# Optimization experiments

Hardware: AMD Instinct MI355X
Metric: run time of the kernel (lower is better)

The kernel has to match this reference:

```python
import jax, jax.numpy as jnp
import numpy as np

N_NODES = 100000
N_EDGES = 3200000
N_FEAT = 512
HIDDEN = 16
N_CLASSES = 40


def gcn_conv(x, src, dst, W, b, num_nodes):
    # GCNConv with self-loops and symmetric normalization (default PyG settings).
    loop = jnp.arange(num_nodes)
    s = jnp.concatenate([src, loop])
    d = jnp.concatenate([dst, loop])
    deg = jax.ops.segment_sum(jnp.ones_like(s, dtype=x.dtype), d, num_segments=num_nodes)
    dinv = jnp.where(deg > 0, jax.lax.rsqrt(deg), 0.0)
    norm = dinv[s] * dinv[d]  # [E+N]
    h = x @ W  # [N, out]
    msg = h[s] * norm[:, None]  # gather + scale
    out = jax.ops.segment_sum(msg, d, num_segments=num_nodes)  # scatter-add
    return out + b


def setup_inputs() -> dict:
    key = jax.random.key(0)
    k1, k2, k3, k4 = jax.random.split(key, 4)
    x = jax.random.normal(k1, (N_NODES, N_FEAT), dtype=jnp.float32)
    edge_index = jax.random.randint(k2, (2, N_EDGES), 0, N_NODES, dtype=jnp.int64)
    W1 = jax.random.normal(k3, (N_FEAT, HIDDEN), dtype=jnp.float32) * 0.05
    b1 = jnp.zeros((HIDDEN,), dtype=jnp.float32)
    W2 = jax.random.normal(k4, (HIDDEN, N_CLASSES), dtype=jnp.float32) * 0.05
    b2 = jnp.zeros((N_CLASSES,), dtype=jnp.float32)
    return {"x": x, "edge_index": edge_index, "W1": W1, "b1": b1, "W2": W2, "b2": b2}


def reference(x, edge_index, W1, b1, W2, b2):
    num_nodes = x.shape[0]
    src, dst = edge_index[0], edge_index[1]
    h = gcn_conv(x, src, dst, W1, b1, num_nodes)
    h = jax.nn.relu(h)
    # dropout is identity in eval mode (training=False)
    out = gcn_conv(h, src, dst, W2, b2, num_nodes)
    return jax.nn.log_softmax(out, axis=1)
```

## Files before the change

kernel.cpp:

```cpp
#include <hip/hip_runtime.h>

#define N_NODES 100000
#define N_EDGES 3200000
#define N_FEAT 512
#define HIDDEN 16
#define N_CLASSES 40

#define SCAN_BLOCKS 98

#define CH3   256
#define NCHK  391
#define NS2   256
#define SLICE2 (N_EDGES / NS2)
#define SL4_2  (SLICE2 / 4)

typedef int v4i __attribute__((ext_vector_type(4)));
typedef int v2i __attribute__((ext_vector_type(2)));

__global__ __launch_bounds__(512) void k_p1b(const int* __restrict__ dst,
                                             int* __restrict__ cnt_sc) {
    __shared__ int hist[NCHK];
    int tid = threadIdx.x;
    int s = blockIdx.x;
    for (int i = tid; i < NCHK; i += 512) hist[i] = 0;
    __syncthreads();
    const v4i* dp = reinterpret_cast<const v4i*>(dst + s * SLICE2);
    for (int i = tid; i < SL4_2; i += 512) {
        v4i d4 = __builtin_nontemporal_load(dp + i);
        atomicAdd(&hist[(unsigned)d4.x >> 8], 1);
        atomicAdd(&hist[(unsigned)d4.y >> 8], 1);
        atomicAdd(&hist[(unsigned)d4.z >> 8], 1);
        atomicAdd(&hist[(unsigned)d4.w >> 8], 1);
    }
    __syncthreads();
    for (int i = tid; i < NCHK; i += 512)
        cnt_sc[s * NCHK + i] = hist[i];
}

__global__ __launch_bounds__(256) void k_scstage2(const int* __restrict__ cnt_sc,
                                                  int* __restrict__ sbase,
                                                  int* __restrict__ tot) {
    int c = blockIdx.x * 4 + (threadIdx.x >> 6);
    int lane = threadIdx.x & 63;
    if (c >= NCHK) return;
    int carry = 0;
    #pragma unroll
    for (int r = 0; r < 4; r++) {
        int s = r * 64 + lane;
        int v = cnt_sc[s * NCHK + c];
        int sc = v;
        #pragma unroll
        for (int off = 1; off < 64; off <<= 1) {
            int t = __shfl_up(sc, off, 64);
            if (lane >= off) sc += t;
        }
        sbase[s * NCHK + c] = carry + sc - v;
        carry += __shfl(sc, 63, 64);
    }
    if (lane == 0) tot[c] = carry;
}

__global__ __launch_bounds__(512) void k_cbscan(const int* __restrict__ tot,
                                                int* __restrict__ cb) {
    int tid = threadIdx.x;
    int v = (tid < NCHK) ? tot[tid] : 0;
    int lane = tid & 63, wv = tid >> 6;
    int sc = v;
    #pragma unroll
    for (int off = 1; off < 64; off <<= 1) {
        int t = __shfl_up(sc, off, 64);
        if (lane >= off) sc += t;
    }
    __shared__ int wsum[8];
    if (lane == 63) wsum[wv] = sc;
    __syncthreads();
    int pre = 0;
    #pragma unroll
    for (int w = 0; w < 8; w++) pre += (w < wv) ? wsum[w] : 0;
    int excl = pre + sc - v;
    if (tid < NCHK) cb[tid] = excl;
    if (tid == NCHK - 1) cb[NCHK] = excl + v;
}

__global__ __launch_bounds__(512) void k_p2stage(const int* __restrict__ src,
                                                 const int* __restrict__ dst,
                                                 const int* __restrict__ sbase,
                                                 const int* __restrict__ cb,
                                                 int2* __restrict__ staged) {
    __shared__ int curpos[NCHK];
    int tid = threadIdx.x;
    int s = blockIdx.x;
    for (int c = tid; c < NCHK; c += 512)
        curpos[c] = cb[c] + sbase[s * NCHK + c];
    __syncthreads();
    const v4i* dp = reinterpret_cast<const v4i*>(dst + s * SLICE2);
    const v4i* sp = reinterpret_cast<const v4i*>(src + s * SLICE2);
    for (int i = tid; i < SL4_2; i += 512) {
        v4i d4 = __builtin_nontemporal_load(dp + i);
        v4i s4 = __builtin_nontemporal_load(sp + i);
        int p0 = atomicAdd(&curpos[(unsigned)d4.x >> 8], 1);
        staged[p0] = make_int2(s4.x, d4.x);
        int p1 = atomicAdd(&curpos[(unsigned)d4.y >> 8], 1);
        staged[p1] = make_int2(s4.y, d4.y);
        int p2 = atomicAdd(&curpos[(unsigned)d4.z >> 8], 1);
        staged[p2] = make_int2(s4.z, d4.z);
        int p3 = atomicAdd(&curpos[(unsigned)d4.w >> 8], 1);
        staged[p3] = make_int2(s4.w, d4.w);
    }
}

__global__ __launch_bounds__(256) void k_deg(const int2* __restrict__ staged,
                                             const int* __restrict__ cb,
                                             int* __restrict__ deg,
                                             float* __restrict__ dinv) {
    __shared__ int cnt[CH3];
    int tid = threadIdx.x;
    int c = blockIdx.x;
    int base = c << 8;
    int lim = N_NODES - base; if (lim > CH3) lim = CH3;
    cnt[tid] = 0;
    __syncthreads();
    int beg = cb[c], end = cb[c + 1];
    const v2i* stp = reinterpret_cast<const v2i*>(staged);
    for (int i = beg + tid; i < end; i += 256) {
        v2i e = stp[i];
        atomicAdd(&cnt[e.y - base], 1);
    }
    __syncthreads();
    if (tid < lim) {
        int d = cnt[tid];
        deg[base + tid] = d;
        dinv[base + tid] = rsqrtf((float)(d + 1));
    }
}


__global__ __launch_bounds__(1024) void k_scan_a(const int* __restrict__ cnt,
                                                 int* __restrict__ bsum) {
    int tid = threadIdx.x;
    int i = blockIdx.x * 1024 + tid;
    int v = (i < N_NODES) ? cnt[i] : 0;
    #pragma unroll
    for (int off = 32; off >= 1; off >>= 1) v += __shfl_xor(v, off, 64);
    __shared__ int ws[16];
    if ((tid & 63) == 0) ws[tid >> 6] = v;
    __syncthreads();
    if (tid == 0) {
        int s = 0;
        #pragma unroll
        for (int w = 0; w < 16; w++) s += ws[w];
        bsum[blockIdx.x] = s;
    }
}

__global__ __launch_bounds__(128) void k_scan_b(const int* __restrict__ bsum,
                                                int* __restrict__ boff) {
    int tid = threadIdx.x;
    int lane = tid & 63, wv = tid >> 6;
    int v = (tid < SCAN_BLOCKS) ? bsum[tid] : 0;
    int sc = v;
    #pragma unroll
    for (int off = 1; off < 64; off <<= 1) {
        int t = __shfl_up(sc, off, 64);
        if (lane >= off) sc += t;
    }
    __shared__ int wsum[2];
    if (lane == 63) wsum[wv] = sc;
    __syncthreads();
    int pre = (wv == 1) ? wsum[0] : 0;
    if (tid < SCAN_BLOCKS) boff[tid] = pre + sc - v;
}

__global__ __launch_bounds__(1024) void k_scan_c(const int* __restrict__ cnt,
                                                 const int* __restrict__ boff,
                                                 int* __restrict__ row_start) {
    int tid = threadIdx.x;
    int i = blockIdx.x * 1024 + tid;
    int lane = tid & 63, wv = tid >> 6;
    int v = (i < N_NODES) ? cnt[i] : 0;
    int sc = v;
    #pragma unroll
    for (int off = 1; off < 64; off <<= 1) {
        int t = __shfl_up(sc, off, 64);
        if (lane >= off) sc += t;
    }
    __shared__ int wsum[16];
    if (lane == 63) wsum[wv] = sc;
    __syncthreads();
    int pre = 0;
    #pragma unroll
    for (int w = 0; w < 16; w++) pre += (w < wv) ? wsum[w] : 0;
    int excl = boff[blockIdx.x] + pre + sc - v;
    if (i < N_NODES) row_start[i] = excl;
    if (i == N_NODES) row_start[N_NODES] = N_EDGES;
}

__global__ __launch_bounds__(512) void k_p3(const int2* __restrict__ staged,
                                            const int* __restrict__ cb,
                                            const int* __restrict__ row_start,
                                            const float* __restrict__ dinv,
                                            int2* __restrict__ edge_data) {
    __shared__ int cur[CH3];
    __shared__ float dv[CH3];
    int tid = threadIdx.x;
    int c = blockIdx.x;
    int base = c << 8;
    int lim = N_NODES - base; if (lim > CH3) lim = CH3;
    if (tid < lim) {
        cur[tid] = row_start[base + tid];
        dv[tid]  = dinv[base + tid];
    }
    __syncthreads();
    int beg = cb[c], end = cb[c + 1];
    const v2i* stp = reinterpret_cast<const v2i*>(staged);
    for (int i = beg + tid; i < end; i += 512) {
        v2i e = __builtin_nontemporal_load(stp + i);
        int nl = e.y - base;
        float nrm = dinv[e.x] * dv[nl];
        int slot = atomicAdd(&cur[nl], 1);
        edge_data[slot] = make_int2(e.x, __float_as_int(nrm));
    }
}


#define KC 32
#define LDSW 36

__global__ __launch_bounds__(256) void k_gemm1(const float* __restrict__ x,
                                               const float* __restrict__ W1,
                                               float* __restrict__ h1) {
    __shared__ float xs[256 * LDSW];
    int tid = threadIdx.x;
    int row = blockIdx.x * 256 + tid;

    float acc[HIDDEN];
    #pragma unroll
    for (int j = 0; j < HIDDEN; j++) acc[j] = 0.f;

    int s_sub = tid >> 3;
    int s_k4  = tid & 7;

    for (int kc = 0; kc < N_FEAT; kc += KC) {
        __syncthreads();
        #pragma unroll
        for (int l = 0; l < 8; l++) {
            int srow = s_sub + l * 32;
            int grow = blockIdx.x * 256 + srow;
            int gr = grow < N_NODES ? grow : N_NODES - 1;
            float4 v = *reinterpret_cast<const float4*>(
                x + (size_t)gr * N_FEAT + kc + s_k4 * 4);
            *reinterpret_cast<float4*>(&xs[srow * LDSW + s_k4 * 4]) = v;
        }
        __syncthreads();

        const float* Wc = W1 + kc * HIDDEN;
        #pragma unroll
        for (int k4 = 0; k4 < 8; k4++) {
            float4 xv = *reinterpret_cast<const float4*>(&xs[tid * LDSW + k4 * 4]);
            const float* w0 = Wc + (k4 * 4 + 0) * HIDDEN;
            const float* w1 = Wc + (k4 * 4 + 1) * HIDDEN;
            const float* w2 = Wc + (k4 * 4 + 2) * HIDDEN;
            const float* w3 = Wc + (k4 * 4 + 3) * HIDDEN;
            #pragma unroll
            for (int j = 0; j < HIDDEN; j++) {
                acc[j] += xv.x * w0[j];
                acc[j] += xv.y * w1[j];
                acc[j] += xv.z * w2[j];
                acc[j] += xv.w * w3[j];
            }
        }
    }

    if (row < N_NODES) {
        float4* op = reinterpret_cast<float4*>(h1 + (size_t)row * HIDDEN);
        #pragma unroll
        for (int q = 0; q < 4; q++)
            op[q] = make_float4(acc[q*4+0], acc[q*4+1], acc[q*4+2], acc[q*4+3]);
    }
}


template <bool RELU>
__global__ __launch_bounds__(256) void k_aggw(const int2* __restrict__ edge_data,
                                              const int* __restrict__ row_start,
                                              const float* __restrict__ dinv,
                                              const float* __restrict__ h,
                                              const float* __restrict__ bias,
                                              float* __restrict__ out) {
    int lane = threadIdx.x & 63;
    int node = blockIdx.x * 4 + (threadIdx.x >> 6);
    int sub = lane >> 4, j = lane & 15;
    int beg = row_start[node], end = row_start[node + 1];
    float ds = dinv[node];
    float acc = (sub == 0) ? h[(size_t)node * HIDDEN + j] * (ds * ds) : 0.f;
    int i = beg + sub;
    for (; i + 12 < end; i += 16) {
        int2 ea = edge_data[i];
        int2 eb = edge_data[i + 4];
        int2 ec = edge_data[i + 8];
        int2 ed = edge_data[i + 12];
        float va = h[(size_t)ea.x * HIDDEN + j];
        float vb = h[(size_t)eb.x * HIDDEN + j];
        float vc = h[(size_t)ec.x * HIDDEN + j];
        float vd = h[(size_t)ed.x * HIDDEN + j];
        acc += va * __int_as_float(ea.y);
        acc += vb * __int_as_float(eb.y);
        acc += vc * __int_as_float(ec.y);
        acc += vd * __int_as_float(ed.y);
    }
    for (; i < end; i += 4) {
        int2 e = edge_data[i];
        acc += h[(size_t)e.x * HIDDEN + j] * __int_as_float(e.y);
    }
    acc += __shfl_xor(acc, 16, 64);
    acc += __shfl_xor(acc, 32, 64);
    if (sub == 0) {
        if (RELU) acc = fmaxf(acc + bias[j], 0.f);
        out[(size_t)node * HIDDEN + j] = acc;
    }
}


__global__ __launch_bounds__(256) void k_out(const float* __restrict__ agg2,
                                             const float* __restrict__ W2,
                                             const float* __restrict__ b2,
                                             float* __restrict__ out) {
    int r = blockIdx.x * 256 + threadIdx.x;
    if (r >= N_NODES) return;
    float a[HIDDEN];
    const float4* ap = reinterpret_cast<const float4*>(agg2 + (size_t)r * HIDDEN);
    #pragma unroll
    for (int q = 0; q < 4; q++) {
        float4 v = ap[q];
        a[q * 4 + 0] = v.x; a[q * 4 + 1] = v.y;
        a[q * 4 + 2] = v.z; a[q * 4 + 3] = v.w;
    }
    float acc[N_CLASSES];
    #pragma unroll
    for (int jj = 0; jj < N_CLASSES; jj++) acc[jj] = b2[jj];
    #pragma unroll
    for (int kk = 0; kk < HIDDEN; kk++) {
        float av = a[kk];
        #pragma unroll
        for (int jj = 0; jj < N_CLASSES; jj++)
            acc[jj] += av * W2[kk * N_CLASSES + jj];
    }
    float m = -1e30f;
    #pragma unroll
    for (int jj = 0; jj < N_CLASSES; jj++) m = fmaxf(m, acc[jj]);
    float sum = 0.f;
    #pragma unroll
    for (int jj = 0; jj < N_CLASSES; jj++) sum += __expf(acc[jj] - m);
    float l = m + __logf(sum);
    float4* op = reinterpret_cast<float4*>(out + (size_t)r * N_CLASSES);
    #pragma unroll
    for (int q = 0; q < N_CLASSES / 4; q++) {
        op[q] = make_float4(acc[q*4+0] - l, acc[q*4+1] - l,
                            acc[q*4+2] - l, acc[q*4+3] - l);
    }
}


extern "C" void kernel_launch(void* const* d_in, const int* in_sizes, int n_in,
                              void* d_out, int out_size, void* d_ws, size_t ws_size,
                              hipStream_t stream) {
    const float* x  = (const float*)d_in[0];
    const int*   ei = (const int*)d_in[1];
    const float* W1 = (const float*)d_in[2];
    const float* b1 = (const float*)d_in[3];
    const float* W2 = (const float*)d_in[4];
    const float* b2 = (const float*)d_in[5];
    const int* src = ei;
    const int* dst = ei + N_EDGES;
    float* out = (float*)d_out;

    char* ws = (char*)d_ws;
    size_t off = 0;
    auto alloc = [&](size_t bytes) {
        size_t o = off; off = (off + bytes + 255) & ~(size_t)255; return o;
    };
    float* dinv      = (float*)(ws + alloc(sizeof(float) * N_NODES));
    int*   cnt       = (int*)  (ws + alloc(sizeof(int) * N_NODES));
    int*   row_start = (int*)  (ws + alloc(sizeof(int) * (N_NODES + 1)));
    int*   cnt_sc    = (int*)  (ws + alloc(sizeof(int) * NS2 * NCHK));
    int*   sbase     = (int*)  (ws + alloc(sizeof(int) * NS2 * NCHK));
    int*   cb        = (int*)  (ws + alloc(sizeof(int) * (NCHK + 1)));
    int*   tot       = (int*)  (ws + alloc(sizeof(int) * NCHK));
    int2*  staged    = (int2*) (ws + alloc(sizeof(int2) * N_EDGES));
    float* h1        = (float*)(ws + off - (size_t)N_EDGES * sizeof(int2));
    float* rbuf      = h1 + (size_t)N_NODES * HIDDEN;
    int2*  edge_data = (int2*) (ws + alloc(sizeof(int2) * N_EDGES));
    float* agg2      = (float*)(ws + alloc(sizeof(float) * N_NODES * HIDDEN));
    int*   bsum      = (int*)  (ws + alloc(sizeof(int) * SCAN_BLOCKS));
    int*   boff      = (int*)  (ws + alloc(sizeof(int) * SCAN_BLOCKS));

    const int nodeBlocks = (N_NODES + 255) / 256;
    const int aggBlocks  = N_NODES / 4;

    k_p1b<<<NS2, 512, 0, stream>>>(dst, cnt_sc);
    k_scstage2<<<(NCHK + 3) / 4, 256, 0, stream>>>(cnt_sc, sbase, tot);
    k_cbscan<<<1, 512, 0, stream>>>(tot, cb);
    k_p2stage<<<NS2, 512, 0, stream>>>(src, dst, sbase, cb, staged);
    k_deg<<<NCHK, 256, 0, stream>>>(staged, cb, cnt, dinv);
    k_scan_a<<<SCAN_BLOCKS, 1024, 0, stream>>>(cnt, bsum);
    k_scan_b<<<1, 128, 0, stream>>>(bsum, boff);
    k_scan_c<<<SCAN_BLOCKS, 1024, 0, stream>>>(cnt, boff, row_start);
    k_p3<<<NCHK, 512, 0, stream>>>(staged, cb, row_start, dinv, edge_data);

    k_gemm1<<<nodeBlocks, 256, 0, stream>>>(x, W1, h1);
    k_aggw<true><<<aggBlocks, 256, 0, stream>>>(edge_data, row_start, dinv, h1, b1, rbuf);
    k_aggw<false><<<aggBlocks, 256, 0, stream>>>(edge_data, row_start, dinv, rbuf, nullptr, agg2);
    k_out<<<nodeBlocks, 256, 0, stream>>>(agg2, W2, b2, out);
}
```

Measured before the change: 571.0 us.

## Fuse CSR-build kernels into one cooperative kernel with grid syncs

Merges the nine graph-preprocessing kernels (histogram, scans, staging, degree, row-start scan, CSR fill) into one cooperative kernel of 256 workgroups, with grid.sync between phases. This removes the launch overhead and inter-kernel gaps of many small kernels. The trade-off is that the degree and CSR-fill phases now run on 256 workgroups looping over 391 chunks instead of 391 blocks, and every grid barrier has its own cost.

```diff
diff --git a/kernel.cpp b/kernel.cpp
--- a/kernel.cpp
+++ b/kernel.cpp
@@ -1,4 +1,7 @@
 #include <hip/hip_runtime.h>
+#include <hip/hip_cooperative_groups.h>
+
+namespace cg = cooperative_groups;
 
 #define N_NODES 100000
 #define N_EDGES 3200000
@@ -6,219 +9,205 @@
 #define HIDDEN 16
 #define N_CLASSES 40
 
-#define SCAN_BLOCKS 98
-
 #define CH3   256
 #define NCHK  391
 #define NS2   256
 #define SLICE2 (N_EDGES / NS2)
 #define SL4_2  (SLICE2 / 4)
+#define RS_WGS 196
 
 typedef int v4i __attribute__((ext_vector_type(4)));
 typedef int v2i __attribute__((ext_vector_type(2)));
 
-__global__ __launch_bounds__(512) void k_p1b(const int* __restrict__ dst,
-                                             int* __restrict__ cnt_sc) {
-    __shared__ int hist[NCHK];
-    int tid = threadIdx.x;
-    int s = blockIdx.x;
-    for (int i = tid; i < NCHK; i += 512) hist[i] = 0;
+__global__ __launch_bounds__(512) void k_build(
+    const int* __restrict__ src, const int* __restrict__ dst,
+    int* __restrict__ cnt_sc, int* __restrict__ sbase, int* __restrict__ tot,
+    int* __restrict__ cb, int* __restrict__ deg, float* __restrict__ dinv,
+    int* __restrict__ bsum, int* __restrict__ boff, int* __restrict__ row_start,
+    int2* __restrict__ staged, int2* __restrict__ edge_data)
+{
+    cg::grid_group grid = cg::this_grid();
+    __shared__ int   sA[NCHK];
+    __shared__ float sB[CH3];
+    const int tid  = threadIdx.x;
+    const int wg   = blockIdx.x;
+    const int lane = tid & 63, wv = tid >> 6;
+
+    for (int i = tid; i < NCHK; i += 512) sA[i] = 0;
     __syncthreads();
-    const v4i* dp = reinterpret_cast<const v4i*>(dst + s * SLICE2);
-    for (int i = tid; i < SL4_2; i += 512) {
-        v4i d4 = __builtin_nontemporal_load(dp + i);
-        atomicAdd(&hist[(unsigned)d4.x >> 8], 1);
-        atomicAdd(&hist[(unsigned)d4.y >> 8], 1);
-        atomicAdd(&hist[(unsigned)d4.z >> 8], 1);
-        atomicAdd(&hist[(unsigned)d4.w >> 8], 1);
-    }
-    __syncthreads();
-    for (int i = tid; i < NCHK; i += 512)
-        cnt_sc[s * NCHK + i] = hist[i];
-}
-
-__global__ __launch_bounds__(256) void k_scstage2(const int* __restrict__ cnt_sc,
-                                                  int* __restrict__ sbase,
-                                                  int* __restrict__ tot) {
-    int c = blockIdx.x * 4 + (threadIdx.x >> 6);
-    int lane = threadIdx.x & 63;
-    if (c >= NCHK) return;
-    int carry = 0;
-    #pragma unroll
-    for (int r = 0; r < 4; r++) {
-        int s = r * 64 + lane;
-        int v = cnt_sc[s * NCHK + c];
+    {
+        const v4i* dp = reinterpret_cast<const v4i*>(dst + wg * SLICE2);
+        for (int i = tid; i < SL4_2; i += 512) {
+            v4i d4 = __builtin_nontemporal_load(dp + i);
+            atomicAdd(&sA[(unsigned)d4.x >> 8], 1);
+            atomicAdd(&sA[(unsigned)d4.y >> 8], 1);
+            atomicAdd(&sA[(unsigned)d4.z >> 8], 1);
+            atomicAdd(&sA[(unsigned)d4.w >> 8], 1);
+        }
+        __syncthreads();
+        for (int i = tid; i < NCHK; i += 512) cnt_sc[wg * NCHK + i] = sA[i];
+    }
+    grid.sync();
+
+    {
+        int c = wg * 8 + wv;
+        if (c < NCHK) {
+            int carry = 0;
+            #pragma unroll
+            for (int r = 0; r < 4; r++) {
+                int s = r * 64 + lane;
+                int v = cnt_sc[s * NCHK + c];
+                int sc = v;
+                #pragma unroll
+                for (int off = 1; off < 64; off <<= 1) {
+                    int t = __shfl_up(sc, off, 64);
+                    if (lane >= off) sc += t;
+                }
+                sbase[s * NCHK + c] = carry + sc - v;
+                carry += __shfl(sc, 63, 64);
+            }
+            if (lane == 0) tot[c] = carry;
+        }
+    }
+    grid.sync();
+
+    if (wg == 0) {
+        int v = (tid < NCHK) ? tot[tid] : 0;
         int sc = v;
         #pragma unroll
         for (int off = 1; off < 64; off <<= 1) {
             int t = __shfl_up(sc, off, 64);
             if (lane >= off) sc += t;
         }
-        sbase[s * NCHK + c] = carry + sc - v;
-        carry += __shfl(sc, 63, 64);
-    }
-    if (lane == 0) tot[c] = carry;
-}
-
-__global__ __launch_bounds__(512) void k_cbscan(const int* __restrict__ tot,
-                                                int* __restrict__ cb) {
-    int tid = threadIdx.x;
-    int v = (tid < NCHK) ? tot[tid] : 0;
-    int lane = tid & 63, wv = tid >> 6;
-    int sc = v;
-    #pragma unroll
-    for (int off = 1; off < 64; off <<= 1) {
-        int t = __shfl_up(sc, off, 64);
-        if (lane >= off) sc += t;
-    }
-    __shared__ int wsum[8];
-    if (lane == 63) wsum[wv] = sc;
-    __syncthreads();
-    int pre = 0;
-    #pragma unroll
-    for (int w = 0; w < 8; w++) pre += (w < wv) ? wsum[w] : 0;
-    int excl = pre + sc - v;
-    if (tid < NCHK) cb[tid] = excl;
-    if (tid == NCHK - 1) cb[NCHK] = excl + v;
-}
-
-__global__ __launch_bounds__(512) void k_p2stage(const int* __restrict__ src,
-                                                 const int* __restrict__ dst,
-                                                 const int* __restrict__ sbase,
-                                                 const int* __restrict__ cb,
-                                                 int2* __restrict__ staged) {
-    __shared__ int curpos[NCHK];
-    int tid = threadIdx.x;
-    int s = blockIdx.x;
-    for (int c = tid; c < NCHK; c += 512)
-        curpos[c] = cb[c] + sbase[s * NCHK + c];
-    __syncthreads();
-    const v4i* dp = reinterpret_cast<const v4i*>(dst + s * SLICE2);
-    const v4i* sp = reinterpret_cast<const v4i*>(src + s * SLICE2);
-    for (int i = tid; i < SL4_2; i += 512) {
-        v4i d4 = __builtin_nontemporal_load(dp + i);
-        v4i s4 = __builtin_nontemporal_load(sp + i);
-        int p0 = atomicAdd(&curpos[(unsigned)d4.x >> 8], 1);
-        staged[p0] = make_int2(s4.x, d4.x);
-        int p1 = atomicAdd(&curpos[(unsigned)d4.y >> 8], 1);
-        staged[p1] = make_int2(s4.y, d4.y);
-        int p2 = atomicAdd(&curpos[(unsigned)d4.z >> 8], 1);
-        staged[p2] = make_int2(s4.z, d4.z);
-        int p3 = atomicAdd(&curpos[(unsigned)d4.w >> 8], 1);
-        staged[p3] = make_int2(s4.w, d4.w);
-    }
-}
-
-__global__ __launch_bounds__(256) void k_deg(const int2* __restrict__ staged,
-                                             const int* __restrict__ cb,
-                                             int* __restrict__ deg,
-                                             float* __restrict__ dinv) {
-    __shared__ int cnt[CH3];
-    int tid = threadIdx.x;
-    int c = blockIdx.x;
-    int base = c << 8;
-    int lim = N_NODES - base; if (lim > CH3) lim = CH3;
-    cnt[tid] = 0;
-    __syncthreads();
-    int beg = cb[c], end = cb[c + 1];
-    const v2i* stp = reinterpret_cast<const v2i*>(staged);
-    for (int i = beg + tid; i < end; i += 256) {
-        v2i e = stp[i];
-        atomicAdd(&cnt[e.y - base], 1);
-    }
-    __syncthreads();
-    if (tid < lim) {
-        int d = cnt[tid];
-        deg[base + tid] = d;
-        dinv[base + tid] = rsqrtf((float)(d + 1));
-    }
-}
-
-
-__global__ __launch_bounds__(1024) void k_scan_a(const int* __restrict__ cnt,
-                                                 int* __restrict__ bsum) {
-    int tid = threadIdx.x;
-    int i = blockIdx.x * 1024 + tid;
-    int v = (i < N_NODES) ? cnt[i] : 0;
-    #pragma unroll
-    for (int off = 32; off >= 1; off >>= 1) v += __shfl_xor(v, off, 64);
-    __shared__ int ws[16];
-    if ((tid & 63) == 0) ws[tid >> 6] = v;
-    __syncthreads();
-    if (tid == 0) {
-        int s = 0;
-        #pragma unroll
-        for (int w = 0; w < 16; w++) s += ws[w];
-        bsum[blockIdx.x] = s;
-    }
-}
-
-__global__ __launch_bounds__(128) void k_scan_b(const int* __restrict__ bsum,
-                                                int* __restrict__ boff) {
-    int tid = threadIdx.x;
-    int lane = tid & 63, wv = tid >> 6;
-    int v = (tid < SCAN_BLOCKS) ? bsum[tid] : 0;
-    int sc = v;
-    #pragma unroll
-    for (int off = 1; off < 64; off <<= 1) {
-        int t = __shfl_up(sc, off, 64);
-        if (lane >= off) sc += t;
-    }
-    __shared__ int wsum[2];
-    if (lane == 63) wsum[wv] = sc;
-    __syncthreads();
-    int pre = (wv == 1) ? wsum[0] : 0;
-    if (tid < SCAN_BLOCKS) boff[tid] = pre + sc - v;
-}
-
-__global__ __launch_bounds__(1024) void k_scan_c(const int* __restrict__ cnt,
-                                                 const int* __restrict__ boff,
-                                                 int* __restrict__ row_start) {
-    int tid = threadIdx.x;
-    int i = blockIdx.x * 1024 + tid;
-    int lane = tid & 63, wv = tid >> 6;
-    int v = (i < N_NODES) ? cnt[i] : 0;
-    int sc = v;
-    #pragma unroll
-    for (int off = 1; off < 64; off <<= 1) {
-        int t = __shfl_up(sc, off, 64);
-        if (lane >= off) sc += t;
-    }
-    __shared__ int wsum[16];
-    if (lane == 63) wsum[wv] = sc;
-    __syncthreads();
-    int pre = 0;
-    #pragma unroll
-    for (int w = 0; w < 16; w++) pre += (w < wv) ? wsum[w] : 0;
-    int excl = boff[blockIdx.x] + pre + sc - v;
-    if (i < N_NODES) row_start[i] = excl;
-    if (i == N_NODES) row_start[N_NODES] = N_EDGES;
-}
-
-__global__ __launch_bounds__(512) void k_p3(const int2* __restrict__ staged,
-                                            const int* __restrict__ cb,
-                                            const int* __restrict__ row_start,
-                                            const float* __restrict__ dinv,
-                                            int2* __restrict__ edge_data) {
-    __shared__ int cur[CH3];
-    __shared__ float dv[CH3];
-    int tid = threadIdx.x;
-    int c = blockIdx.x;
-    int base = c << 8;
-    int lim = N_NODES - base; if (lim > CH3) lim = CH3;
-    if (tid < lim) {
-        cur[tid] = row_start[base + tid];
-        dv[tid]  = dinv[base + tid];
-    }
-    __syncthreads();
-    int beg = cb[c], end = cb[c + 1];
-    const v2i* stp = reinterpret_cast<const v2i*>(staged);
-    for (int i = beg + tid; i < end; i += 512) {
-        v2i e = __builtin_nontemporal_load(stp + i);
-        int nl = e.y - base;
-        float nrm = dinv[e.x] * dv[nl];
-        int slot = atomicAdd(&cur[nl], 1);
-        edge_data[slot] = make_int2(e.x, __float_as_int(nrm));
+        if (lane == 63) sA[wv] = sc;
+        __syncthreads();
+        int pre = 0;
+        #pragma unroll
+        for (int w = 0; w < 8; w++) pre += (w < wv) ? sA[w] : 0;
+        int excl = pre + sc - v;
+        if (tid < NCHK) cb[tid] = excl;
+        if (tid == NCHK - 1) cb[NCHK] = excl + v;
+    }
+    grid.sync();
+
+    {
+        for (int c = tid; c < NCHK; c += 512)
+            sA[c] = cb[c] + sbase[wg * NCHK + c];
+        __syncthreads();
+        const v4i* dp = reinterpret_cast<const v4i*>(dst + wg * SLICE2);
+        const v4i* sp = reinterpret_cast<const v4i*>(src + wg * SLICE2);
+        for (int i = tid; i < SL4_2; i += 512) {
+            v4i d4 = __builtin_nontemporal_load(dp + i);
+            v4i s4 = __builtin_nontemporal_load(sp + i);
+            int p0 = atomicAdd(&sA[(unsigned)d4.x >> 8], 1);
+            staged[p0] = make_int2(s4.x, d4.x);
+            int p1 = atomicAdd(&sA[(unsigned)d4.y >> 8], 1);
+            staged[p1] = make_int2(s4.y, d4.y);
+            int p2 = atomicAdd(&sA[(unsigned)d4.z >> 8], 1);
+            staged[p2] = make_int2(s4.z, d4.z);
+            int p3 = atomicAdd(&sA[(unsigned)d4.w >> 8], 1);
+            staged[p3] = make_int2(s4.w, d4.w);
+        }
+    }
+    grid.sync();
+
+    for (int c = wg; c < NCHK; c += NS2) {
+        int base = c << 8;
+        int lim = N_NODES - base; if (lim > CH3) lim = CH3;
+        if (tid < CH3) sA[tid] = 0;
+        __syncthreads();
+        int beg = cb[c], end = cb[c + 1];
+        const v2i* stp = reinterpret_cast<const v2i*>(staged);
+        for (int i = beg + tid; i < end; i += 512) {
+            v2i e = stp[i];
+            atomicAdd(&sA[e.y - base], 1);
+        }
+        __syncthreads();
+        if (tid < lim) {
+            int d = sA[tid];
+            deg[base + tid] = d;
+            dinv[base + tid] = rsqrtf((float)(d + 1));
+        }
+        __syncthreads();
+    }
+    grid.sync();
+
+    if (wg < RS_WGS) {
+        int i = wg * 512 + tid;
+        int v = (i < N_NODES) ? deg[i] : 0;
+        int sc = v;
+        #pragma unroll
+        for (int off = 1; off < 64; off <<= 1) {
+            int t = __shfl_up(sc, off, 64);
+            if (lane >= off) sc += t;
+        }
+        if (lane == 63) sA[wv] = sc;
+        __syncthreads();
+        if (tid == 0) {
+            int t8 = 0;
+            #pragma unroll
+            for (int w = 0; w < 8; w++) t8 += sA[w];
+            bsum[wg] = t8;
+        }
+    }
+    grid.sync();
+
+    if (wg == 0) {
+        int v = (tid < RS_WGS) ? bsum[tid] : 0;
+        int sc = v;
+        #pragma unroll
+        for (int off = 1; off < 64; off <<= 1) {
+            int t = __shfl_up(sc, off, 64);
+            if (lane >= off) sc += t;
+        }
+        if (lane == 63) sA[wv] = sc;
+        __syncthreads();
+        int pre = 0;
+        #pragma unroll
+        for (int w = 0; w < 8; w++) pre += (w < wv) ? sA[w] : 0;
+        if (tid < RS_WGS) boff[tid] = pre + sc - v;
+    }
+    grid.sync();
+
+    if (wg < RS_WGS) {
+        int i = wg * 512 + tid;
+        int v = (i < N_NODES) ? deg[i] : 0;
+        int sc = v;
+        #pragma unroll
+        for (int off = 1; off < 64; off <<= 1) {
+            int t = __shfl_up(sc, off, 64);
+            if (lane >= off) sc += t;
+        }
+        if (lane == 63) sA[wv] = sc;
+        __syncthreads();
+        int pre = 0;
+        #pragma unroll
+        for (int w = 0; w < 8; w++) pre += (w < wv) ? sA[w] : 0;
+        int excl = pre + sc - v;
+        if (i < N_NODES) row_start[i] = boff[wg] + excl;
+        if (i == N_NODES) row_start[N_NODES] = N_EDGES;
+        __syncthreads();
+    }
+    grid.sync();
+
+    for (int c = wg; c < NCHK; c += NS2) {
+        int base = c << 8;
+        int lim = N_NODES - base; if (lim > CH3) lim = CH3;
+        if (tid < lim) {
+            sA[tid] = row_start[base + tid];
+            sB[tid] = dinv[base + tid];
+        }
+        __syncthreads();
+        int beg = cb[c], end = cb[c + 1];
+        const v2i* stp = reinterpret_cast<const v2i*>(staged);
+        for (int i = beg + tid; i < end; i += 512) {
+            v2i e = __builtin_nontemporal_load(stp + i);
+            int nl = e.y - base;
+            float nrm = dinv[e.x] * sB[nl];
+            int slot = atomicAdd(&sA[nl], 1);
+            edge_data[slot] = make_int2(e.x, __float_as_int(nrm));
+        }
+        __syncthreads();
     }
 }
 
@@ -391,21 +380,18 @@
     float* rbuf      = h1 + (size_t)N_NODES * HIDDEN;
     int2*  edge_data = (int2*) (ws + alloc(sizeof(int2) * N_EDGES));
     float* agg2      = (float*)(ws + alloc(sizeof(float) * N_NODES * HIDDEN));
-    int*   bsum      = (int*)  (ws + alloc(sizeof(int) * SCAN_BLOCKS));
-    int*   boff      = (int*)  (ws + alloc(sizeof(int) * SCAN_BLOCKS));
+    int*   bsum      = (int*)  (ws + alloc(sizeof(int) * RS_WGS));
+    int*   boff      = (int*)  (ws + alloc(sizeof(int) * RS_WGS));
 
     const int nodeBlocks = (N_NODES + 255) / 256;
     const int aggBlocks  = N_NODES / 4;
 
-    k_p1b<<<NS2, 512, 0, stream>>>(dst, cnt_sc);
-    k_scstage2<<<(NCHK + 3) / 4, 256, 0, stream>>>(cnt_sc, sbase, tot);
-    k_cbscan<<<1, 512, 0, stream>>>(tot, cb);
-    k_p2stage<<<NS2, 512, 0, stream>>>(src, dst, sbase, cb, staged);
-    k_deg<<<NCHK, 256, 0, stream>>>(staged, cb, cnt, dinv);
-    k_scan_a<<<SCAN_BLOCKS, 1024, 0, stream>>>(cnt, bsum);
-    k_scan_b<<<1, 128, 0, stream>>>(bsum, boff);
-    k_scan_c<<<SCAN_BLOCKS, 1024, 0, stream>>>(cnt, boff, row_start);
-    k_p3<<<NCHK, 512, 0, stream>>>(staged, cb, row_start, dinv, edge_data);
+    void* args[] = {(void*)&src, (void*)&dst, (void*)&cnt_sc, (void*)&sbase,
+                    (void*)&tot, (void*)&cb, (void*)&cnt, (void*)&dinv,
+                    (void*)&bsum, (void*)&boff, (void*)&row_start,
+                    (void*)&staged, (void*)&edge_data};
+    hipLaunchCooperativeKernel(reinterpret_cast<void*>(k_build),
+                               dim3(NS2), dim3(512), args, 0, stream);
 
     k_gemm1<<<nodeBlocks, 256, 0, stream>>>(x, W1, h1);
     k_aggw<true><<<aggBlocks, 256, 0, stream>>>(edge_data, row_start, dinv, h1, b1, rbuf);
```

Result: slower. 789.5 us (+38.3%).
